# Performance work log

Measured on AMD Instinct MI355X. Metric: run time of the kernel, lower is better.

Reference implementation:

```python
import jax, jax.numpy as jnp
import numpy as np

N = 500000   # number of points
C = 64       # in_channels == out_channels
L = 4        # n_layers


def setup_inputs() -> dict:
    key = jax.random.key(0)
    ks = jax.random.split(key, 7)
    s = np.float32(1.0 / np.sqrt(C))  # keep activations O(1) across layers
    return {
        "features": jax.random.normal(ks[0], (N, C), jnp.float32),
        "points": jax.random.normal(ks[1], (N, 3), jnp.float32),
        "nuv": jax.random.normal(ks[2], (N, 3, 3), jnp.float32),
        "W0": jax.random.normal(ks[3], (L, C, C), jnp.float32) * s,  # linear_transform
        "b0": jnp.zeros((L, C), jnp.float32),
        "W1": jax.random.normal(ks[4], (L, C, C), jnp.float32) * s,  # linear_block[0]
        "b1": jnp.zeros((L, C), jnp.float32),
        "W2": jax.random.normal(ks[5], (L, C, C), jnp.float32) * s,  # linear_block[2]
        "b2": jnp.zeros((L, C), jnp.float32),
    }


def reference(features, points, nuv, W0, b0, W1, b1, W2, b2):
    # Faithful to the torch source: inside each DMaSIFConvBlock the dmasif_conv
    # output is overwritten by linear_transform(features), so the effective math
    # per block is: x = Linear2(relu(Linear1(Linear0(x)))).
    # points / nuv / ranges do not influence the output.
    del points, nuv

    def step(x, params):
        w0, c0, w1, c1, w2, c2 = params
        h = x @ w0 + c0                      # linear_transform
        h = jax.nn.relu(h @ w1 + c1)          # linear_block: Linear + ReLU
        h = h @ w2 + c2                      # linear_block: Linear
        return h, None

    out, _ = jax.lax.scan(step, features, (W0, b0, W1, b1, W2, b2))
    return out
```

## Files before the change

kernel.cpp:

```cpp
#include <hip/hip_runtime.h>
#include <stdint.h>

#define CH 64
#define NPTS 500000
#define NW 7813
#define NSTEP 12
#define BLK 256
#define WPB (BLK / 64)

typedef float floatx16 __attribute__((ext_vector_type(16)));
typedef __bf16 bf16x8 __attribute__((ext_vector_type(8)));

__device__ __forceinline__ unsigned pk(float odd, float even) {
    return __builtin_amdgcn_perm(__float_as_uint(odd), __float_as_uint(even), 0x07060302u);
}
__device__ __forceinline__ float hif(float x) {
    return __uint_as_float(__float_as_uint(x) & 0xffff0000u);
}

struct U16 { unsigned a, b, c, d; };
__device__ __forceinline__ bf16x8 asb4(unsigned x0, unsigned x1, unsigned x2, unsigned x3) {
    U16 t{x0, x1, x2, x3};
    return __builtin_bit_cast(bf16x8, t);
}
__device__ __forceinline__ bf16x8 asbu4(uint4 v) {
    return __builtin_bit_cast(bf16x8, v);
}

typedef __attribute__((address_space(3))) void lds_void;
typedef const __attribute__((address_space(1))) void gm_void;
__device__ __forceinline__ void gload_lds16(const void* g, void* l) {
    __builtin_amdgcn_global_load_lds((gm_void*)g, (lds_void*)l, 16, 0, 0);
}

#define MFMA_B(A, Bv, C) __builtin_amdgcn_mfma_f32_32x32x16_bf16(asbu4(A), Bv, C, 0, 0, 0)

__global__ void prep_weights(const float* __restrict__ W0,
                             const float* __restrict__ W1,
                             const float* __restrict__ W2,
                             uint4* __restrict__ wsA) {
    const int g  = blockIdx.x * blockDim.x + threadIdx.x;
    const int mp = g & 31;
    const int h  = (g >> 5) & 1;
    const int q  = (g >> 6) & 3;
    const int mt = (g >> 8) & 1;
    const int pl = (g >> 9) & 1;
    const int s  = g >> 10;
    const float* Wb = (s % 3 == 0) ? W0 : ((s % 3 == 1) ? W1 : W2);
    const float* Ws = Wb + (s / 3) * CH * CH;
    const int m   = mt * 32 + mp;
    const int col = (m & ~12) | ((m & 4) << 1) | ((m & 8) >> 1);
    unsigned o[4];
    #pragma unroll
    for (int d = 0; d < 4; ++d) {
        float e = Ws[(16 * q + 8 * h + 2 * d) * CH + col];
        float v = Ws[(16 * q + 8 * h + 2 * d + 1) * CH + col];
        if (pl) { e = e - hif(e); v = v - hif(v); }
        o[d] = pk(v, e);
    }
    wsA[g] = make_uint4(o[0], o[1], o[2], o[3]);
}

__global__ __launch_bounds__(BLK, 2) void mlp12_mfma(
    const float* __restrict__ feat,
    const uint4* __restrict__ wsA,
    const float* __restrict__ b0,
    const float* __restrict__ b1,
    const float* __restrict__ b2,
    float* __restrict__ out)
{
    __shared__ uint4 sA[2][1024];

    const int tid  = threadIdx.x;
    const int lane = tid & 63;
    const int wv   = tid >> 6;
    int wid = blockIdx.x * WPB + wv;
    if (wid > NW - 1) wid = NW - 1;
    const int n = lane & 31;
    const int h = lane >> 5;
    const size_t row0 = ((size_t)wid * 64 + n) * CH;
    const size_t row1 = (wid == NW - 1) ? row0 : row0 + (size_t)32 * CH;

    {
        const char* g = (const char*)wsA;
        #pragma unroll
        for (int c = 0; c < 4; ++c)
            gload_lds16(g + (wv * 4 + c) * 1024 + lane * 16,
                        (char*)&sA[0][0] + (wv * 4 + c) * 1024);
    }

    unsigned Bhi[2][4][4], Blo[2][4][4];
    {
        const float* f0 = feat + row0 + 8 * h;
        const float* f1 = feat + row1 + 8 * h;
        #pragma unroll
        for (int q = 0; q < 4; ++q) {
            float4 va = *(const float4*)(f0 + 16 * q);
            float4 vb = *(const float4*)(f0 + 16 * q + 4);
            Bhi[0][q][0] = pk(va.y, va.x);  Bhi[0][q][1] = pk(va.w, va.z);
            Bhi[0][q][2] = pk(vb.y, vb.x);  Bhi[0][q][3] = pk(vb.w, vb.z);
            Blo[0][q][0] = pk(va.y - hif(va.y), va.x - hif(va.x));
            Blo[0][q][1] = pk(va.w - hif(va.w), va.z - hif(va.z));
            Blo[0][q][2] = pk(vb.y - hif(vb.y), vb.x - hif(vb.x));
            Blo[0][q][3] = pk(vb.w - hif(vb.w), vb.z - hif(vb.z));
            float4 vc = *(const float4*)(f1 + 16 * q);
            float4 vd = *(const float4*)(f1 + 16 * q + 4);
            Bhi[1][q][0] = pk(vc.y, vc.x);  Bhi[1][q][1] = pk(vc.w, vc.z);
            Bhi[1][q][2] = pk(vd.y, vd.x);  Bhi[1][q][3] = pk(vd.w, vd.z);
            Blo[1][q][0] = pk(vc.y - hif(vc.y), vc.x - hif(vc.x));
            Blo[1][q][1] = pk(vc.w - hif(vc.w), vc.z - hif(vc.z));
            Blo[1][q][2] = pk(vd.y - hif(vd.y), vd.x - hif(vd.x));
            Blo[1][q][3] = pk(vd.w - hif(vd.w), vd.z - hif(vd.z));
        }
    }
    __syncthreads();

    floatx16 ac00, ac01, ac10, ac11;

    #pragma unroll 1
    for (int k = 0; k < 2; ++k) {
        const char*  gk  = (const char*)wsA + (size_t)k * 6 * 16384;
        const float* bb0 = b0 + 2 * k * CH;
        const float* bb1 = b1 + 2 * k * CH;
        const float* bb2 = b2 + 2 * k * CH;
        #pragma unroll
        for (int j = 0; j < 6; ++j) {
            const int s = 6 * k + j;
            const int b = j & 1;

            if (s + 1 < NSTEP) {
                const char* g = gk + (size_t)(j + 1) * 16384;
                #pragma unroll
                for (int c = 0; c < 4; ++c)
                    gload_lds16(g + (wv * 4 + c) * 1024 + lane * 16,
                                (char*)&sA[1 - b][0] + (wv * 4 + c) * 1024);
            }

            const uint4* base = &sA[b][0];

            uint4 Acur[4], Anx[4];
            #pragma unroll
            for (int t = 0; t < 4; ++t) Acur[t] = base[(t * 4 + 0) * 64 + lane];

            if (s > 0) {
                const bool relu = (j % 3 == 2);
                #pragma unroll
                for (int q = 0; q < 4; ++q) {
                    const int rr = q & 1;
                    #pragma unroll
                    for (int d = 0; d < 4; ++d) {
                        float e, o;
                        if (q < 2) { e = ac00[8*rr+2*d]; o = ac00[8*rr+2*d+1]; }
                        else       { e = ac01[8*rr+2*d]; o = ac01[8*rr+2*d+1]; }
                        if (relu) { e = fmaxf(e, 0.f); o = fmaxf(o, 0.f); }
                        Bhi[0][q][d] = pk(o, e);
                        Blo[0][q][d] = pk(o - hif(o), e - hif(e));
                    }
                }
                #pragma unroll
                for (int q = 0; q < 4; ++q) {
                    const int rr = q & 1;
                    #pragma unroll
                    for (int d = 0; d < 4; ++d) {
                        float e, o;
                        if (q < 2) { e = ac10[8*rr+2*d]; o = ac10[8*rr+2*d+1]; }
                        else       { e = ac11[8*rr+2*d]; o = ac11[8*rr+2*d+1]; }
                        if (relu) { e = fmaxf(e, 0.f); o = fmaxf(o, 0.f); }
                        Bhi[1][q][d] = pk(o, e);
                        Blo[1][q][d] = pk(o - hif(o), e - hif(e));
                    }
                }
            }

            {
                const float* bs = ((j % 3 == 0) ? bb0 : (j % 3 == 1) ? bb1 : bb2)
                                  + (j / 3) * CH;
                #pragma unroll
                for (int rq = 0; rq < 4; ++rq) {
                    const int off = 16 * (rq >> 1) + 8 * h + 4 * (rq & 1);
                    float4 v0 = *(const float4*)(bs + off);
                    float4 v1 = *(const float4*)(bs + 32 + off);
                    ac00[4*rq+0] = v0.x; ac00[4*rq+1] = v0.y;
                    ac00[4*rq+2] = v0.z; ac00[4*rq+3] = v0.w;
                    ac10[4*rq+0] = v0.x; ac10[4*rq+1] = v0.y;
                    ac10[4*rq+2] = v0.z; ac10[4*rq+3] = v0.w;
                    ac01[4*rq+0] = v1.x; ac01[4*rq+1] = v1.y;
                    ac01[4*rq+2] = v1.z; ac01[4*rq+3] = v1.w;
                    ac11[4*rq+0] = v1.x; ac11[4*rq+1] = v1.y;
                    ac11[4*rq+2] = v1.z; ac11[4*rq+3] = v1.w;
                }
            }

            #pragma unroll
            for (int q = 0; q < 4; ++q) {
                if (q < 3) {
                    #pragma unroll
                    for (int t = 0; t < 4; ++t) Anx[t] = base[(t * 4 + q + 1) * 64 + lane];
                }
                bf16x8 b0h = asb4(Bhi[0][q][0], Bhi[0][q][1], Bhi[0][q][2], Bhi[0][q][3]);
                bf16x8 b0l = asb4(Blo[0][q][0], Blo[0][q][1], Blo[0][q][2], Blo[0][q][3]);
                bf16x8 b1h = asb4(Bhi[1][q][0], Bhi[1][q][1], Bhi[1][q][2], Bhi[1][q][3]);
                bf16x8 b1l = asb4(Blo[1][q][0], Blo[1][q][1], Blo[1][q][2], Blo[1][q][3]);
                ac00 = MFMA_B(Acur[0], b0h, ac00);
                ac01 = MFMA_B(Acur[1], b0h, ac01);
                ac10 = MFMA_B(Acur[0], b1h, ac10);
                ac11 = MFMA_B(Acur[1], b1h, ac11);
                ac00 = MFMA_B(Acur[2], b0h, ac00);
                ac01 = MFMA_B(Acur[3], b0h, ac01);
                ac10 = MFMA_B(Acur[2], b1h, ac10);
                ac11 = MFMA_B(Acur[3], b1h, ac11);
                ac00 = MFMA_B(Acur[0], b0l, ac00);
                ac01 = MFMA_B(Acur[1], b0l, ac01);
                ac10 = MFMA_B(Acur[0], b1l, ac10);
                ac11 = MFMA_B(Acur[1], b1l, ac11);
                #pragma unroll
                for (int t = 0; t < 4; ++t) Acur[t] = Anx[t];
            }

            __syncthreads();
        }
    }

    float* o0 = out + row0;
    float* o1 = out + row1;
    #pragma unroll
    for (int rq = 0; rq < 4; ++rq) {
        const int off = 16 * (rq >> 1) + 8 * h + 4 * (rq & 1);
        float4 v;
        v.x = ac00[4*rq+0]; v.y = ac00[4*rq+1]; v.z = ac00[4*rq+2]; v.w = ac00[4*rq+3];
        *(float4*)(o0 + off) = v;
        v.x = ac01[4*rq+0]; v.y = ac01[4*rq+1]; v.z = ac01[4*rq+2]; v.w = ac01[4*rq+3];
        *(float4*)(o0 + 32 + off) = v;
        v.x = ac10[4*rq+0]; v.y = ac10[4*rq+1]; v.z = ac10[4*rq+2]; v.w = ac10[4*rq+3];
        *(float4*)(o1 + off) = v;
        v.x = ac11[4*rq+0]; v.y = ac11[4*rq+1]; v.z = ac11[4*rq+2]; v.w = ac11[4*rq+3];
        *(float4*)(o1 + 32 + off) = v;
    }
}

extern "C" void kernel_launch(void* const* d_in, const int* in_sizes, int n_in,
                              void* d_out, int out_size, void* d_ws, size_t ws_size,
                              hipStream_t stream) {
    const float* feat = (const float*)d_in[0];
    const float* W0 = (const float*)d_in[3];
    const float* b0 = (const float*)d_in[4];
    const float* W1 = (const float*)d_in[5];
    const float* b1 = (const float*)d_in[6];
    const float* W2 = (const float*)d_in[7];
    const float* b2 = (const float*)d_in[8];
    float* out = (float*)d_out;
    uint4* wsA = (uint4*)d_ws;

    prep_weights<<<48, 256, 0, stream>>>(W0, W1, W2, wsA);

    const int grid = (NW + WPB - 1) / WPB;
    mlp12_mfma<<<grid, BLK, 0, stream>>>(feat, wsA, b0, b1, b2, out);
}
```

Measured before the change: 339.0 us.

## Load weight fragments directly from global memory instead of LDS staging

```diff
diff --git a/kernel.cpp b/kernel.cpp
--- a/kernel.cpp
+++ b/kernel.cpp
@@ -25,12 +25,6 @@
 }
 __device__ __forceinline__ bf16x8 asbu4(uint4 v) {
     return __builtin_bit_cast(bf16x8, v);
-}
-
-typedef __attribute__((address_space(3))) void lds_void;
-typedef const __attribute__((address_space(1))) void gm_void;
-__device__ __forceinline__ void gload_lds16(const void* g, void* l) {
-    __builtin_amdgcn_global_load_lds((gm_void*)g, (lds_void*)l, 16, 0, 0);
 }
 
 #define MFMA_B(A, Bv, C) __builtin_amdgcn_mfma_f32_32x32x16_bf16(asbu4(A), Bv, C, 0, 0, 0)
@@ -69,25 +63,21 @@
     const float* __restrict__ b2,
     float* __restrict__ out)
 {
-    __shared__ uint4 sA[2][1024];
-
     const int tid  = threadIdx.x;
     const int lane = tid & 63;
     const int wv   = tid >> 6;
-    int wid = blockIdx.x * WPB + wv;
-    if (wid > NW - 1) wid = NW - 1;
+    const int wid  = blockIdx.x * WPB + wv;
+    if (wid >= NW) return;
     const int n = lane & 31;
     const int h = lane >> 5;
     const size_t row0 = ((size_t)wid * 64 + n) * CH;
     const size_t row1 = (wid == NW - 1) ? row0 : row0 + (size_t)32 * CH;
 
-    {
-        const char* g = (const char*)wsA;
-        #pragma unroll
-        for (int c = 0; c < 4; ++c)
-            gload_lds16(g + (wv * 4 + c) * 1024 + lane * 16,
-                        (char*)&sA[0][0] + (wv * 4 + c) * 1024);
-    }
+    const uint4* wlane = wsA + lane;
+
+    uint4 Acur[4], Anx[4];
+    #pragma unroll
+    for (int t = 0; t < 4; ++t) Acur[t] = wlane[(t * 4) * 64];
 
     unsigned Bhi[2][4][4], Blo[2][4][4];
     {
@@ -113,34 +103,18 @@
             Blo[1][q][3] = pk(vd.w - hif(vd.w), vd.z - hif(vd.z));
         }
     }
-    __syncthreads();
 
     floatx16 ac00, ac01, ac10, ac11;
 
     #pragma unroll 1
     for (int k = 0; k < 2; ++k) {
-        const char*  gk  = (const char*)wsA + (size_t)k * 6 * 16384;
         const float* bb0 = b0 + 2 * k * CH;
         const float* bb1 = b1 + 2 * k * CH;
         const float* bb2 = b2 + 2 * k * CH;
         #pragma unroll
         for (int j = 0; j < 6; ++j) {
             const int s = 6 * k + j;
-            const int b = j & 1;
-
-            if (s + 1 < NSTEP) {
-                const char* g = gk + (size_t)(j + 1) * 16384;
-                #pragma unroll
-                for (int c = 0; c < 4; ++c)
-                    gload_lds16(g + (wv * 4 + c) * 1024 + lane * 16,
-                                (char*)&sA[1 - b][0] + (wv * 4 + c) * 1024);
-            }
-
-            const uint4* base = &sA[b][0];
-
-            uint4 Acur[4], Anx[4];
-            #pragma unroll
-            for (int t = 0; t < 4; ++t) Acur[t] = base[(t * 4 + 0) * 64 + lane];
+            const uint4* base = wlane + (size_t)s * 1024;
 
             if (s > 0) {
                 const bool relu = (j % 3 == 2);
@@ -195,7 +169,10 @@
             for (int q = 0; q < 4; ++q) {
                 if (q < 3) {
                     #pragma unroll
-                    for (int t = 0; t < 4; ++t) Anx[t] = base[(t * 4 + q + 1) * 64 + lane];
+                    for (int t = 0; t < 4; ++t) Anx[t] = base[(t * 4 + q + 1) * 64];
+                } else if (s + 1 < NSTEP) {
+                    #pragma unroll
+                    for (int t = 0; t < 4; ++t) Anx[t] = base[(t * 4) * 64 + 1024];
                 }
                 bf16x8 b0h = asb4(Bhi[0][q][0], Bhi[0][q][1], Bhi[0][q][2], Bhi[0][q][3]);
                 bf16x8 b0l = asb4(Blo[0][q][0], Blo[0][q][1], Blo[0][q][2], Blo[0][q][3]);
@@ -216,8 +193,6 @@
                 #pragma unroll
                 for (int t = 0; t < 4; ++t) Acur[t] = Anx[t];
             }
-
-            __syncthreads();
         }
     }
 
```

Measured after the change: 369.5 us. 1.09x slower.
